# Optimization experiments

Hardware: AMD Instinct MI355X
Metric: run time of the kernel (lower is better)

The kernel has to match this reference:

```python
import jax, jax.numpy as jnp
import numpy as np

N = 100000   # nodes
E = 1600000  # edges
D = 128      # d_model
FF = 512     # dim_feedforward
EPS = 1e-5


def setup_inputs() -> dict:
    key = jax.random.key(0)
    ks = jax.random.split(key, 12)
    x = jax.random.normal(ks[0], (N, D), dtype=jnp.float32)
    edge_index = jax.random.randint(ks[1], (2, E), 0, N, dtype=jnp.int64)
    edge_weight = jax.random.uniform(ks[2], (E,), dtype=jnp.float32)
    sD = 1.0 / np.sqrt(D)
    sFF = 1.0 / np.sqrt(FF)
    W = jax.random.normal(ks[3], (D, D), dtype=jnp.float32) * sD   # GCN weight
    b = jnp.zeros((D,), jnp.float32)                                # GCN bias
    gamma = jnp.ones((D,), jnp.float32)                             # shared batchnorm
    beta = jnp.zeros((D,), jnp.float32)
    W1 = jax.random.normal(ks[4], (D, FF), dtype=jnp.float32) * sD  # MLP lin1
    b1 = jnp.zeros((FF,), jnp.float32)
    W2 = jax.random.normal(ks[5], (FF, D), dtype=jnp.float32) * sFF # MLP lin2
    b2 = jnp.zeros((D,), jnp.float32)
    return {"x": x, "edge_index": edge_index, "edge_weight": edge_weight,
            "W": W, "b": b, "gamma": gamma, "beta": beta,
            "W1": W1, "b1": b1, "W2": W2, "b2": b2}


def gcn_conv(x, edge_index, edge_weight, W, b):
    # GCNConv with add_self_loops=True (self-loop weight 1) and symmetric norm.
    h = x @ W                                   # [N, D]
    src, dst = edge_index[0], edge_index[1]
    deg = jax.ops.segment_sum(edge_weight, dst, num_segments=N) + 1.0
    dinv = jnp.where(deg > 0, jax.lax.rsqrt(deg), 0.0)
    norm = dinv[src] * edge_weight * dinv[dst]  # [E]
    out = jax.ops.segment_sum(norm[:, None] * h[src], dst, num_segments=N)
    out = out + (dinv * dinv)[:, None] * h      # self-loop contribution
    return out + b


def batch_norm(x, gamma, beta):
    # training-mode BatchNorm1d over the node (batch) dimension
    mu = jnp.mean(x, axis=0)
    var = jnp.mean((x - mu) ** 2, axis=0)
    return gamma * (x - mu) * jax.lax.rsqrt(var + EPS) + beta


def reference(x, edge_index, edge_weight, W, b, gamma, beta, W1, b1, W2, b2):
    x1 = batch_norm(x + gcn_conv(x, edge_index, edge_weight, W, b), gamma, beta)
    x2 = jax.nn.relu(x1 @ W1 + b1) @ W2 + b2    # MLP d_model->dim_ff->d_model
    return batch_norm(x1 + x2, gamma, beta)
```

## Files before the change

### kernel.cpp

```cpp
#include <hip/hip_runtime.h>

#define NN 100000
#define EE 1600000
#define DD 128
#define FFD 512
#define EPSV 1e-5f

#define SCB 98

typedef __attribute__((ext_vector_type(8))) short bf16x8;
typedef __attribute__((ext_vector_type(4))) float f32x4;
typedef unsigned long long ull;

__device__ __forceinline__ ushort f2b(float f) {
    uint u = __float_as_uint(f);
    return (ushort)((u + 0x7FFF + ((u >> 16) & 1)) >> 16);
}
__device__ __forceinline__ float b2f(ushort u) {
    return __uint_as_float(((uint)u) << 16);
}


__global__ __launch_bounds__(256) void k_init(ull* pk, float* s1, float* s2) {
    int i = blockIdx.x * 256 + threadIdx.x;
    if (i < NN) pk[i] = 0ULL;
    if (blockIdx.x == 0) { s1[threadIdx.x] = 0.f; s2[threadIdx.x] = 0.f; }
}


__global__ __launch_bounds__(256) void k_edge_deg(const int* __restrict__ ei,
                                                  const float* __restrict__ ew,
                                                  ull* __restrict__ pk,
                                                  int* __restrict__ rank) {
    int e = blockIdx.x * 256 + threadIdx.x;
    if (e < EE) {
        int dst = ei[EE + e];
        uint fx = (uint)(ew[e] * 16777216.0f + 0.5f);
        ull old = atomicAdd(&pk[dst], (1ULL << 32) | (ull)fx);
        rank[e] = (int)(old >> 32);
    }
}


__global__ __launch_bounds__(256) void k_scan_part(const ull* __restrict__ pk,
                                                   int* __restrict__ cnt,
                                                   float* __restrict__ dinv,
                                                   int* __restrict__ bsum) {
    __shared__ int red[4];
    int b = blockIdx.x, t = threadIdx.x;
    int base = b * 1024 + t * 4;
    int s = 0;
#pragma unroll
    for (int j = 0; j < 4; ++j) {
        int i = base + j;
        if (i < NN) {
            ull v = pk[i];
            int c = (int)(v >> 32);
            cnt[i] = c;
            dinv[i] = rsqrtf(1.0f + (float)(uint)(v & 0xFFFFFFFFu) * (1.0f / 16777216.0f));
            s += c;
        }
    }
#pragma unroll
    for (int d = 1; d < 64; d <<= 1) s += __shfl_xor(s, d);
    if ((t & 63) == 0) red[t >> 6] = s;
    __syncthreads();
    if (t == 0) bsum[b] = red[0] + red[1] + red[2] + red[3];
}

__global__ __launch_bounds__(128) void k_scan_base(int* __restrict__ bsum,
                                                   int* __restrict__ bbase,
                                                   int* __restrict__ start) {
    if (threadIdx.x == 0) {
        int run = 0;
        for (int i = 0; i < SCB; ++i) { bbase[i] = run; run += bsum[i]; }
        start[NN] = run;
    }
}

__global__ __launch_bounds__(256) void k_scan_fin(const int* __restrict__ cnt,
                                                  const int* __restrict__ bbase,
                                                  int* __restrict__ start) {
    __shared__ int ts[256];
    int b = blockIdx.x, t = threadIdx.x;
    int base = b * 1024 + t * 4;
    int v[4];
    int s = 0;
#pragma unroll
    for (int j = 0; j < 4; ++j) {
        int i = base + j;
        v[j] = (i < NN) ? cnt[i] : 0;
        s += v[j];
    }
    ts[t] = s;
    __syncthreads();
    for (int d = 1; d < 256; d <<= 1) {
        int add = (t >= d) ? ts[t - d] : 0;
        __syncthreads();
        ts[t] += add;
        __syncthreads();
    }
    int run = bbase[b] + ts[t] - s;
#pragma unroll
    for (int j = 0; j < 4; ++j) {
        int i = base + j;
        if (i < NN) {
            start[i] = run;
            run += v[j];
        }
    }
}


__global__ __launch_bounds__(256) void k_fill(const int* __restrict__ ei,
                                              const float* __restrict__ ew,
                                              const float* __restrict__ dinv,
                                              const int* __restrict__ start,
                                              const int* __restrict__ rank,
                                              uint2* __restrict__ csr) {
    int e = blockIdx.x * 256 + threadIdx.x;
    if (e < EE) {
        int src = ei[e];
        int dst = ei[EE + e];
        float nrm = dinv[src] * ew[e] * dinv[dst];
        int pos = start[dst] + rank[e];
        csr[pos] = make_uint2((uint)src, __float_as_uint(nrm));
    }
}


__global__ __launch_bounds__(256) void k_wcvt(const float* __restrict__ W,
                                              const float* __restrict__ W1,
                                              const float* __restrict__ W2,
                                              ushort* __restrict__ WTb,
                                              ushort* __restrict__ W1Tb,
                                              ushort* __restrict__ W2Tb) {
    int i = blockIdx.x * 256 + threadIdx.x;
    if (i < 16384) {
        int n = i >> 7, k = i & 127;
        WTb[i] = f2b(W[k * 128 + n]);
    } else if (i < 16384 + 65536) {
        int j = i - 16384;
        int f = j >> 7, k = j & 127;
        W1Tb[j] = f2b(W1[k * 512 + f]);
    } else {
        int j = i - 16384 - 65536;
        int jj = j >> 9, f = j & 511;
        W2Tb[j] = f2b(W2[f * 128 + jj]);
    }
}


__global__ __launch_bounds__(256) void k_xb(const float* __restrict__ x,
                                            ushort* __restrict__ xb) {
    long i = (long)blockIdx.x * 256 + threadIdx.x;
    float4 v = ((const float4*)x)[i];
    ushort4 o;
    o.x = f2b(v.x); o.y = f2b(v.y); o.z = f2b(v.z); o.w = f2b(v.w);
    ((ushort4*)xb)[i] = o;
}


__global__ __launch_bounds__(256) void k_gather(const ushort* __restrict__ xb,
                                                const float* __restrict__ dinv,
                                                const int* __restrict__ start,
                                                const uint2* __restrict__ csr,
                                                ushort* __restrict__ aggx) {
    int t = threadIdx.x;
    int wv = t >> 6, l = t & 63;
    const uint* xbu = (const uint*)xb;
    uint* aggu = (uint*)aggx;

    for (int k = 0; k < 8; ++k) {
        int node = blockIdx.x * 32 + wv * 8 + k;
        int e0 = start[node], e1 = start[node + 1];
        float a0 = 0.f, a1 = 0.f;
        int i = e0;
        for (; i + 8 <= e1; i += 8) {
            uint2 rr[8];
            uint hh[8];
#pragma unroll
            for (int u = 0; u < 8; ++u) rr[u] = csr[i + u];
#pragma unroll
            for (int u = 0; u < 8; ++u) hh[u] = xbu[rr[u].x * 64 + l];
#pragma unroll
            for (int u = 0; u < 8; ++u) {
                float n = __uint_as_float(rr[u].y);
                a0 = fmaf(n, b2f((ushort)(hh[u] & 0xFFFF)), a0);
                a1 = fmaf(n, b2f((ushort)(hh[u] >> 16)), a1);
            }
        }
        if (i + 4 <= e1) {
            uint2 rr[4];
            uint hh[4];
#pragma unroll
            for (int u = 0; u < 4; ++u) rr[u] = csr[i + u];
#pragma unroll
            for (int u = 0; u < 4; ++u) hh[u] = xbu[rr[u].x * 64 + l];
#pragma unroll
            for (int u = 0; u < 4; ++u) {
                float n = __uint_as_float(rr[u].y);
                a0 = fmaf(n, b2f((ushort)(hh[u] & 0xFFFF)), a0);
                a1 = fmaf(n, b2f((ushort)(hh[u] >> 16)), a1);
            }
            i += 4;
        }
        for (; i < e1; ++i) {
            uint2 r0 = csr[i];
            uint h0 = xbu[r0.x * 64 + l];
            float n0 = __uint_as_float(r0.y);
            a0 = fmaf(n0, b2f((ushort)(h0 & 0xFFFF)), a0);
            a1 = fmaf(n0, b2f((ushort)(h0 >> 16)), a1);
        }
        float dv = dinv[node];
        float sl = dv * dv;
        uint hs = xbu[node * 64 + l];
        a0 = fmaf(sl, b2f((ushort)(hs & 0xFFFF)), a0);
        a1 = fmaf(sl, b2f((ushort)(hs >> 16)), a1);
        aggu[node * 64 + l] = (uint)f2b(a0) | ((uint)f2b(a1) << 16);
    }
}


__global__ __launch_bounds__(256) void k_conv(const float* __restrict__ x,
                                              const ushort* __restrict__ aggx,
                                              const ushort* __restrict__ WTb,
                                              const float* __restrict__ b,
                                              ushort* __restrict__ yb,
                                              float* __restrict__ stats1) {
    __shared__ __align__(16) ushort xt[64][136];
    __shared__ __align__(16) ushort wt[128][136];
    int t = threadIdx.x;
    int row0 = blockIdx.x * 64;

    for (int i = t; i < 2048; i += 256) {
        int r = i >> 4, c8 = (i & 15) << 3;
        *(uint4*)&wt[r][c8] = ((const uint4*)WTb)[i];
    }
    for (int i = t; i < 1024; i += 256) {
        int r = i >> 4, c8 = (i & 15) << 3;
        int gr = row0 + r;
        uint4 v = make_uint4(0u, 0u, 0u, 0u);
        if (gr < NN) v = ((const uint4*)aggx)[(long)gr * 16 + (i & 15)];
        *(uint4*)&xt[r][c8] = v;
    }
    __syncthreads();

    int wv = t >> 6, l = t & 63;
    int lr = l & 15, lg = l >> 4;
    int rw = wv & 1, jw = wv >> 1;

    f32x4 z4 = {0.f, 0.f, 0.f, 0.f};
    f32x4 acc[4][2];
#pragma unroll
    for (int jt = 0; jt < 4; ++jt)
#pragma unroll
        for (int rt = 0; rt < 2; ++rt) acc[jt][rt] = z4;

#pragma unroll
    for (int ks = 0; ks < 4; ++ks) {
        bf16x8 qR0 = *(const bf16x8*)&xt[rw * 32 + lr][ks * 32 + lg * 8];
        bf16x8 qR1 = *(const bf16x8*)&xt[rw * 32 + 16 + lr][ks * 32 + lg * 8];
#pragma unroll
        for (int jt = 0; jt < 4; ++jt) {
            bf16x8 pW = *(const bf16x8*)&wt[jw * 64 + jt * 16 + lr][ks * 32 + lg * 8];
            acc[jt][0] = __builtin_amdgcn_mfma_f32_16x16x32_bf16(pW, qR0, acc[jt][0], 0, 0, 0);
            acc[jt][1] = __builtin_amdgcn_mfma_f32_16x16x32_bf16(pW, qR1, acc[jt][1], 0, 0, 0);
        }
    }

    float sj[4][4], qj[4][4];
#pragma unroll
    for (int jt = 0; jt < 4; ++jt)
#pragma unroll
        for (int g = 0; g < 4; ++g) { sj[jt][g] = 0.f; qj[jt][g] = 0.f; }

#pragma unroll
    for (int jt = 0; jt < 4; ++jt) {
        int jb = jw * 64 + jt * 16 + lg * 4;
        float4 bv = *(const float4*)&b[jb];
#pragma unroll
        for (int rt = 0; rt < 2; ++rt) {
            int rloc = rw * 32 + rt * 16 + lr;
            int r = row0 + rloc;
            if (r < NN) {
                float4 xv = *(const float4*)&x[(long)r * 128 + jb];
                float z0 = xv.x + acc[jt][rt][0] + bv.x;
                float z1 = xv.y + acc[jt][rt][1] + bv.y;
                float z2 = xv.z + acc[jt][rt][2] + bv.z;
                float z3 = xv.w + acc[jt][rt][3] + bv.w;
                ushort4 o;
                o.x = f2b(z0); o.y = f2b(z1); o.z = f2b(z2); o.w = f2b(z3);
                *(ushort4*)&yb[(long)r * 128 + jb] = o;
                sj[jt][0] += z0; sj[jt][1] += z1; sj[jt][2] += z2; sj[jt][3] += z3;
                qj[jt][0] += z0 * z0; qj[jt][1] += z1 * z1; qj[jt][2] += z2 * z2; qj[jt][3] += z3 * z3;
            }
        }
    }
#pragma unroll
    for (int jt = 0; jt < 4; ++jt)
#pragma unroll
        for (int g = 0; g < 4; ++g) {
#pragma unroll
            for (int d = 1; d < 16; d <<= 1) {
                sj[jt][g] += __shfl_xor(sj[jt][g], d);
                qj[jt][g] += __shfl_xor(qj[jt][g], d);
            }
        }
    __syncthreads();
    float* redS = (float*)&xt[0][0];
    float* redQ = redS + 512;
    if (lr == 0) {
#pragma unroll
        for (int jt = 0; jt < 4; ++jt)
#pragma unroll
            for (int g = 0; g < 4; ++g) {
                int j = jw * 64 + jt * 16 + lg * 4 + g;
                redS[wv * 128 + j] = sj[jt][g];
                redQ[wv * 128 + j] = qj[jt][g];
            }
    }
    __syncthreads();
    if (t < 128) {
        int w0 = (t >> 6) * 2;
        atomicAdd(&stats1[t], redS[w0 * 128 + t] + redS[(w0 + 1) * 128 + t]);
        atomicAdd(&stats1[128 + t], redQ[w0 * 128 + t] + redQ[(w0 + 1) * 128 + t]);
    }
}


__global__ __launch_bounds__(128) void k_bn_fin(const float* __restrict__ stats,
                                                const float* __restrict__ gamma,
                                                const float* __restrict__ beta,
                                                float* __restrict__ ac) {
    int c = threadIdx.x;
    float mu = stats[c] * (1.0f / NN);
    float var = stats[128 + c] * (1.0f / NN) - mu * mu;
    float a = gamma[c] * rsqrtf(var + EPSV);
    ac[c] = a;
    ac[128 + c] = beta[c] - mu * a;
}

__global__ __launch_bounds__(256) void k_affine(float* __restrict__ v,
                                                const float* __restrict__ ac) {
    long i = (long)blockIdx.x * 256 + threadIdx.x;
    int c4i = (int)(i & 31);
    float4 a = ((const float4*)ac)[c4i];
    float4 cc = ((const float4*)(ac + 128))[c4i];
    float4 v4 = ((float4*)v)[i];
    v4.x = a.x * v4.x + cc.x;
    v4.y = a.y * v4.y + cc.y;
    v4.z = a.z * v4.z + cc.z;
    v4.w = a.w * v4.w + cc.w;
    ((float4*)v)[i] = v4;
}


#define SWZ(row, kb) ((((kb) ^ ((row) & 7)) << 3))

__global__ __launch_bounds__(256, 3) void k_mlp(const ushort* __restrict__ yb,
                                                const float* __restrict__ ac1,
                                                const ushort* __restrict__ W1Tb,
                                                const float* __restrict__ b1,
                                                const ushort* __restrict__ W2Tb,
                                                const float* __restrict__ b2,
                                                float* __restrict__ out,
                                                float* __restrict__ stats2) {
    __shared__ __align__(16) ushort xt[32 * 128];
    __shared__ __align__(16) ushort ht[32 * 128];
    __shared__ __align__(16) ushort wc[128 * 128];
    int t = threadIdx.x;
    int row0 = blockIdx.x * 32;

    for (int i = t; i < 512; i += 256) {
        int r = i >> 4, kb = i & 15;
        long base = (long)(row0 + r) * 32 + kb * 2;
        ushort4 y0 = ((const ushort4*)yb)[base];
        ushort4 y1 = ((const ushort4*)yb)[base + 1];
        float4 a0 = ((const float4*)ac1)[kb * 2];
        float4 a1 = ((const float4*)ac1)[kb * 2 + 1];
        float4 c0 = ((const float4*)(ac1 + 128))[kb * 2];
        float4 c1 = ((const float4*)(ac1 + 128))[kb * 2 + 1];
        ushort4 o0, o1;
        o0.x = f2b(a0.x * b2f(y0.x) + c0.x);
        o0.y = f2b(a0.y * b2f(y0.y) + c0.y);
        o0.z = f2b(a0.z * b2f(y0.z) + c0.z);
        o0.w = f2b(a0.w * b2f(y0.w) + c0.w);
        o1.x = f2b(a1.x * b2f(y1.x) + c1.x);
        o1.y = f2b(a1.y * b2f(y1.y) + c1.y);
        o1.z = f2b(a1.z * b2f(y1.z) + c1.z);
        o1.w = f2b(a1.w * b2f(y1.w) + c1.w);
        ushort* dst = &xt[r * 128 + SWZ(r, kb)];
        *(ushort4*)dst = o0;
        *(ushort4*)(dst + 4) = o1;
    }

    int wv = t >> 6, l = t & 63;
    int lr = l & 15, lg = l >> 4;
    int rw = wv & 1, jw = wv >> 1;
    int xrow = rw * 16 + lr;
    int s7 = lr & 7;

    f32x4 z4 = {0.f, 0.f, 0.f, 0.f};
    f32x4 acc[4];
#pragma unroll
    for (int jt = 0; jt < 4; ++jt) acc[jt] = z4;

    for (int ch = 0; ch < 4; ++ch) {
        __syncthreads();
        for (int i = t; i < 2048; i += 256) {
            int f = i >> 4, kb = i & 15;
            uint4 v = ((const uint4*)W1Tb)[(ch * 128 + f) * 16 + kb];
            *(uint4*)&wc[f * 128 + SWZ(f, kb)] = v;
        }
        __syncthreads();

        f32x4 hacc[4];
#pragma unroll
        for (int ft = 0; ft < 4; ++ft) hacc[ft] = z4;
#pragma unroll
        for (int ks = 0; ks < 4; ++ks) {
            int kcol = ((ks * 4 + lg) ^ s7) << 3;
            bf16x8 aR = *(const bf16x8*)&xt[xrow * 128 + kcol];
#pragma unroll
            for (int ft = 0; ft < 4; ++ft) {
                int f = jw * 64 + ft * 16 + lr;
                bf16x8 bW = *(const bf16x8*)&wc[f * 128 + kcol];
                hacc[ft] = __builtin_amdgcn_mfma_f32_16x16x32_bf16(aR, bW, hacc[ft], 0, 0, 0);
            }
        }
#pragma unroll
        for (int ft = 0; ft < 4; ++ft) {
            int fcol = jw * 64 + ft * 16 + lr;
            float b1v = b1[ch * 128 + fcol];
            int kbf = fcol >> 3, wi = fcol & 7;
#pragma unroll
            for (int rg = 0; rg < 4; ++rg) {
                int hrow = rw * 16 + lg * 4 + rg;
                ht[hrow * 128 + ((kbf ^ (hrow & 7)) << 3) + wi] =
                    f2b(fmaxf(hacc[ft][rg] + b1v, 0.f));
            }
        }
        __syncthreads();

        for (int i = t; i < 2048; i += 256) {
            int j = i >> 4, kb = i & 15;
            uint4 v = ((const uint4*)W2Tb)[j * 64 + ch * 16 + kb];
            *(uint4*)&wc[j * 128 + SWZ(j, kb)] = v;
        }
        __syncthreads();

#pragma unroll
        for (int ks = 0; ks < 4; ++ks) {
            int kcol = ((ks * 4 + lg) ^ s7) << 3;
            bf16x8 qR = *(const bf16x8*)&ht[xrow * 128 + kcol];
#pragma unroll
            for (int jt = 0; jt < 4; ++jt) {
                int j = jw * 64 + jt * 16 + lr;
                bf16x8 pW = *(const bf16x8*)&wc[j * 128 + kcol];
                acc[jt] = __builtin_amdgcn_mfma_f32_16x16x32_bf16(pW, qR, acc[jt], 0, 0, 0);
            }
        }
    }

    float sj[4][4], qj[4][4];
    int r = row0 + xrow;
#pragma unroll
    for (int jt = 0; jt < 4; ++jt) {
        int jb = jw * 64 + jt * 16 + lg * 4;
        float4 b2v = *(const float4*)&b2[jb];
        int kbj = jb >> 3, wj = jb & 7;
        ushort4 xv = *(const ushort4*)&xt[xrow * 128 + ((kbj ^ s7) << 3) + wj];
        float z0 = b2f(xv.x) + acc[jt][0] + b2v.x;
        float z1 = b2f(xv.y) + acc[jt][1] + b2v.y;
        float z2 = b2f(xv.z) + acc[jt][2] + b2v.z;
        float z3 = b2f(xv.w) + acc[jt][3] + b2v.w;
        *(float4*)&out[(long)r * 128 + jb] = make_float4(z0, z1, z2, z3);
        sj[jt][0] = z0; sj[jt][1] = z1; sj[jt][2] = z2; sj[jt][3] = z3;
        qj[jt][0] = z0 * z0; qj[jt][1] = z1 * z1; qj[jt][2] = z2 * z2; qj[jt][3] = z3 * z3;
    }
#pragma unroll
    for (int jt = 0; jt < 4; ++jt)
#pragma unroll
        for (int g = 0; g < 4; ++g) {
#pragma unroll
            for (int d = 1; d < 16; d <<= 1) {
                sj[jt][g] += __shfl_xor(sj[jt][g], d);
                qj[jt][g] += __shfl_xor(qj[jt][g], d);
            }
        }
    __syncthreads();
    float* redS = (float*)&ht[0];
    float* redQ = redS + 512;
    if (lr == 0) {
#pragma unroll
        for (int jt = 0; jt < 4; ++jt)
#pragma unroll
            for (int g = 0; g < 4; ++g) {
                int j = jw * 64 + jt * 16 + lg * 4 + g;
                redS[wv * 128 + j] = sj[jt][g];
                redQ[wv * 128 + j] = qj[jt][g];
            }
    }
    __syncthreads();
    if (t < 128) {
        int w0 = (t >> 6) * 2;
        atomicAdd(&stats2[t], redS[w0 * 128 + t] + redS[(w0 + 1) * 128 + t]);
        atomicAdd(&stats2[128 + t], redQ[w0 * 128 + t] + redQ[(w0 + 1) * 128 + t]);
    }
}


extern "C" void kernel_launch(void* const* d_in, const int* in_sizes, int n_in,
                              void* d_out, int out_size, void* d_ws, size_t ws_size,
                              hipStream_t stream) {
    const float* x     = (const float*)d_in[0];
    const int*   ei    = (const int*)d_in[1];
    const float* ew    = (const float*)d_in[2];
    const float* W     = (const float*)d_in[3];
    const float* b     = (const float*)d_in[4];
    const float* gamma = (const float*)d_in[5];
    const float* beta  = (const float*)d_in[6];
    const float* W1    = (const float*)d_in[7];
    const float* b1    = (const float*)d_in[8];
    const float* W2    = (const float*)d_in[9];
    const float* b2    = (const float*)d_in[10];
    float* out = (float*)d_out;
    float* ws  = (float*)d_ws;

    ull*   pk     = (ull*)ws;
    float* dinv   = ws + 2 * NN;
    float* stats1 = ws + 3 * NN;
    float* ac1    = stats1 + 256;
    float* stats2 = ac1 + 256;
    float* ac2    = stats2 + 256;
    ushort* xb    = (ushort*)(ws + 3 * NN + 1024);
    ushort* WTb   = xb + (long)NN * 128;
    ushort* W1Tb  = WTb + 16384;
    ushort* W2Tb  = W1Tb + 65536;
    float*  fend  = ws + 3 * NN + 1024 + (long)NN * 64 + 73728;
    int*   cnt    = (int*)fend;
    int*   start  = cnt + NN;
    int*   bsum   = start + NN + 1;
    int*   bbase  = bsum + SCB;
    uint2* csr    = (uint2*)(((uintptr_t)(bbase + SCB) + 7) & ~(uintptr_t)7);
    ushort* aggx  = (ushort*)(csr + EE);
    int*   rank   = (int*)aggx;
    ushort* yb    = xb;

    int nb = (NN + 63) / 64;

    k_init<<<(NN + 255) / 256, 256, 0, stream>>>(pk, stats1, stats2);
    k_edge_deg<<<EE / 256, 256, 0, stream>>>(ei, ew, pk, rank);
    k_scan_part<<<SCB, 256, 0, stream>>>(pk, cnt, dinv, bsum);
    k_scan_base<<<1, 128, 0, stream>>>(bsum, bbase, start);
    k_scan_fin<<<SCB, 256, 0, stream>>>(cnt, bbase, start);
    k_fill<<<EE / 256, 256, 0, stream>>>(ei, ew, dinv, start, rank, csr);
    k_wcvt<<<576, 256, 0, stream>>>(W, W1, W2, WTb, W1Tb, W2Tb);
    k_xb<<<(NN * 32) / 256, 256, 0, stream>>>(x, xb);
    k_gather<<<NN / 32, 256, 0, stream>>>(xb, dinv, start, csr, aggx);
    k_conv<<<nb, 256, 0, stream>>>(x, aggx, WTb, b, yb, stats1);
    k_bn_fin<<<1, 128, 0, stream>>>(stats1, gamma, beta, ac1);
    k_mlp<<<NN / 32, 256, 0, stream>>>(yb, ac1, W1Tb, b1, W2Tb, b2, out, stats2);
    k_bn_fin<<<1, 128, 0, stream>>>(stats2, gamma, beta, ac2);
    k_affine<<<(NN * 32) / 256, 256, 0, stream>>>(out, ac2);
}
```

Baseline: 397.6 us.

## Register-prefetch MLP weight tiles and widen LDS swizzle to 16 rows

The MLP kernel now loads the next W1/W2 weight chunk from global memory into registers while the current chunk is being consumed, then writes it to shared memory. This overlaps global loads with MFMA compute instead of stalling on each load-then-store loop. The XOR swizzle is also widened from 8 to 16 rows to reduce LDS bank conflicts. The cost is 32 extra VGPRs per thread for the prefetch buffer, which may reduce occupancy under the 3-blocks-per-SM launch bound, plus an extra barrier per iteration.

```diff
diff --git a/kernel.cpp b/kernel.cpp
--- a/kernel.cpp
+++ b/kernel.cpp
@@ -356,7 +356,7 @@
 }
 
 
-#define SWZ(row, kb) ((((kb) ^ ((row) & 7)) << 3))
+#define SWZ16(row, kb) ((((kb) ^ ((row) & 15)) << 3))
 
 __global__ __launch_bounds__(256, 3) void k_mlp(const ushort* __restrict__ yb,
                                                 const float* __restrict__ ac1,
@@ -371,6 +371,12 @@
     __shared__ __align__(16) ushort wc[128 * 128];
     int t = threadIdx.x;
     int row0 = blockIdx.x * 32;
+    int f0 = t >> 4, kb0 = t & 15;
+
+    uint4 wR[8];
+#pragma unroll
+    for (int j = 0; j < 8; ++j)
+        wR[j] = ((const uint4*)W1Tb)[(f0 + j * 16) * 16 + kb0];
 
     for (int i = t; i < 512; i += 256) {
         int r = i >> 4, kb = i & 15;
@@ -390,7 +396,7 @@
         o1.y = f2b(a1.y * b2f(y1.y) + c1.y);
         o1.z = f2b(a1.z * b2f(y1.z) + c1.z);
         o1.w = f2b(a1.w * b2f(y1.w) + c1.w);
-        ushort* dst = &xt[r * 128 + SWZ(r, kb)];
+        ushort* dst = &xt[r * 128 + SWZ16(r, kb)];
         *(ushort4*)dst = o0;
         *(ushort4*)(dst + 4) = o1;
     }
@@ -399,28 +405,31 @@
     int lr = l & 15, lg = l >> 4;
     int rw = wv & 1, jw = wv >> 1;
     int xrow = rw * 16 + lr;
-    int s7 = lr & 7;
 
     f32x4 z4 = {0.f, 0.f, 0.f, 0.f};
     f32x4 acc[4];
 #pragma unroll
     for (int jt = 0; jt < 4; ++jt) acc[jt] = z4;
 
+    __syncthreads();
+
     for (int ch = 0; ch < 4; ++ch) {
+#pragma unroll
+        for (int j = 0; j < 8; ++j) {
+            int f = f0 + j * 16;
+            *(uint4*)&wc[f * 128 + SWZ16(f, kb0)] = wR[j];
+        }
+#pragma unroll
+        for (int j = 0; j < 8; ++j)
+            wR[j] = ((const uint4*)W2Tb)[(f0 + j * 16) * 64 + ch * 16 + kb0];
         __syncthreads();
-        for (int i = t; i < 2048; i += 256) {
-            int f = i >> 4, kb = i & 15;
-            uint4 v = ((const uint4*)W1Tb)[(ch * 128 + f) * 16 + kb];
-            *(uint4*)&wc[f * 128 + SWZ(f, kb)] = v;
-        }
-        __syncthreads();
 
         f32x4 hacc[4];
 #pragma unroll
         for (int ft = 0; ft < 4; ++ft) hacc[ft] = z4;
 #pragma unroll
         for (int ks = 0; ks < 4; ++ks) {
-            int kcol = ((ks * 4 + lg) ^ s7) << 3;
+            int kcol = ((ks * 4 + lg) ^ lr) << 3;
             bf16x8 aR = *(const bf16x8*)&xt[xrow * 128 + kcol];
 #pragma unroll
             for (int ft = 0; ft < 4; ++ft) {
@@ -437,22 +446,27 @@
 #pragma unroll
             for (int rg = 0; rg < 4; ++rg) {
                 int hrow = rw * 16 + lg * 4 + rg;
-                ht[hrow * 128 + ((kbf ^ (hrow & 7)) << 3) + wi] =
+                ht[hrow * 128 + ((kbf ^ (hrow & 15)) << 3) + wi] =
                     f2b(fmaxf(hacc[ft][rg] + b1v, 0.f));
             }
         }
         __syncthreads();
 
-        for (int i = t; i < 2048; i += 256) {
-            int j = i >> 4, kb = i & 15;
-            uint4 v = ((const uint4*)W2Tb)[j * 64 + ch * 16 + kb];
-            *(uint4*)&wc[j * 128 + SWZ(j, kb)] = v;
+#pragma unroll
+        for (int j = 0; j < 8; ++j) {
+            int f = f0 + j * 16;
+            *(uint4*)&wc[f * 128 + SWZ16(f, kb0)] = wR[j];
+        }
+        if (ch < 3) {
+#pragma unroll
+            for (int j = 0; j < 8; ++j)
+                wR[j] = ((const uint4*)W1Tb)[((ch + 1) * 128 + f0 + j * 16) * 16 + kb0];
         }
         __syncthreads();
 
 #pragma unroll
         for (int ks = 0; ks < 4; ++ks) {
-            int kcol = ((ks * 4 + lg) ^ s7) << 3;
+            int kcol = ((ks * 4 + lg) ^ lr) << 3;
             bf16x8 qR = *(const bf16x8*)&ht[xrow * 128 + kcol];
 #pragma unroll
             for (int jt = 0; jt < 4; ++jt) {
@@ -461,6 +475,7 @@
                 acc[jt] = __builtin_amdgcn_mfma_f32_16x16x32_bf16(pW, qR, acc[jt], 0, 0, 0);
             }
         }
+        __syncthreads();
     }
 
     float sj[4][4], qj[4][4];
@@ -470,7 +485,7 @@
         int jb = jw * 64 + jt * 16 + lg * 4;
         float4 b2v = *(const float4*)&b2[jb];
         int kbj = jb >> 3, wj = jb & 7;
-        ushort4 xv = *(const ushort4*)&xt[xrow * 128 + ((kbj ^ s7) << 3) + wj];
+        ushort4 xv = *(const ushort4*)&xt[xrow * 128 + ((kbj ^ lr) << 3) + wj];
         float z0 = b2f(xv.x) + acc[jt][0] + b2v.x;
         float z1 = b2f(xv.y) + acc[jt][1] + b2v.y;
         float z2 = b2f(xv.z) + acc[jt][2] + b2v.z;
```

Measured after the change: 522.7 us. 31.5% more time.
